# Optimization experiments

Hardware: AMD Instinct MI355X
Metric: run time of the kernel (lower is better)

## Reference

```python
import jax, jax.numpy as jnp
import numpy as np

V, E, H, B, T = 50000, 300, 512, 256, 64
D_OUT = 3
EPS = 1e-5


def setup_inputs() -> dict:
    key = jax.random.key(0)
    ks = jax.random.split(key, 16)
    s = lambda k, shape: (jax.random.normal(k, shape, jnp.float32) * 0.05)
    return {
        "premise": jax.random.randint(ks[0], (T, B), 0, V),
        "hypothesis": jax.random.randint(ks[1], (T, B), 0, V),
        "embed": s(ks[2], (V, E)),
        "W_ih": s(ks[3], (4 * H, E)),
        "W_hh": s(ks[4], (4 * H, H)),
        "b_ih": s(ks[5], (4 * H,)),
        "b_hh": s(ks[6], (4 * H,)),
        "bn0_g": jnp.ones((4 * H,), jnp.float32),
        "bn0_b": jnp.zeros((4 * H,), jnp.float32),
        "W0": s(ks[7], (4 * H, 4 * H)),
        "b0": s(ks[8], (4 * H,)),
        "bn1_g": jnp.ones((4 * H,), jnp.float32),
        "bn1_b": jnp.zeros((4 * H,), jnp.float32),
        "W1": s(ks[9], (4 * H, 4 * H)),
        "b1": s(ks[10], (4 * H,)),
        "bno_g": jnp.ones((4 * H,), jnp.float32),
        "bno_b": jnp.zeros((4 * H,), jnp.float32),
        "Wo": s(ks[11], (D_OUT, 4 * H)),
        "bo": s(ks[12], (D_OUT,)),
    }


def _lstm_final_h(xs, W_ih, W_hh, bias):
    # xs: [T, N, E]; shared-weight LSTMCell scan, returns final hidden [N, H]
    x_proj = jnp.einsum('tne,ge->tng', xs, W_ih) + bias  # hoist input GEMM out of the recurrence
    n = xs.shape[1]
    h0 = jnp.zeros((n, H), xs.dtype)

    def step(carry, xg):
        h, c = carry
        gates = xg + h @ W_hh.T
        i, f, g, o = jnp.split(gates, 4, axis=-1)  # torch LSTMCell gate order
        c = jax.nn.sigmoid(f) * c + jax.nn.sigmoid(i) * jnp.tanh(g)
        h = jax.nn.sigmoid(o) * jnp.tanh(c)
        return (h, c), None

    (h, _), _ = jax.lax.scan(step, (h0, h0), x_proj)
    return h


def _bn(x, g, b):
    # BatchNorm1d in training mode: biased batch stats
    mu = x.mean(0)
    var = x.var(0)
    return (x - mu) * jax.lax.rsqrt(var + EPS) * g + b


def reference(premise, hypothesis, embed, W_ih, W_hh, b_ih, b_hh,
              bn0_g, bn0_b, W0, b0, bn1_g, bn1_b, W1, b1,
              bno_g, bno_b, Wo, bo):
    p = embed[premise]      # [T, B, E]
    hyp = embed[hypothesis]  # [T, B, E]
    combined = jnp.concatenate([p, hyp], axis=1)  # [T, 2B, E]
    bias = b_ih + b_hh
    h_fw = _lstm_final_h(combined, W_ih, W_hh, bias)          # forward direction
    h_bw = _lstm_final_h(combined[::-1], W_ih, W_hh, bias)    # backward direction (shared cell)
    feat = jnp.concatenate([h_fw[:B], h_bw[:B], h_fw[B:], h_bw[B:]], axis=1)  # [B, 4H]
    x = jax.nn.relu(_bn(feat, bn0_g, bn0_b) @ W0.T + b0)
    x = jax.nn.relu(_bn(x, bn1_g, bn1_b) @ W1.T + b1)
    return _bn(x, bno_g, bno_b) @ Wo.T + bo  # [B, d_out]
```

## Files before the change

kernel.cpp:

```cpp
#include <hip/hip_runtime.h>
#include <hip/hip_bf16.h>


typedef __attribute__((ext_vector_type(8))) short bf16x8;
typedef __attribute__((ext_vector_type(4))) float f32x4;
typedef __attribute__((ext_vector_type(2))) unsigned int u32x2;

#define DEVI __device__ __forceinline__

template<int N> struct IC { static constexpr int v = N; };

template<int AUX> DEVI void async16t(const void* g, void* l) {
  __builtin_amdgcn_global_load_lds((const __attribute__((address_space(1))) void*)g,
                                   (__attribute__((address_space(3))) void*)l,
                                   16, 0, AUX);
}
DEVI void async16(const void* g, void* l) { async16t<0>(g, l); }
DEVI u32x2 load8_pin(const void* addr) {
  u32x2 r;
  asm volatile("global_load_dwordx2 %0, %1, off" : "=v"(r) : "v"(addr) : "memory");
  return r;
}
DEVI void storeh_coh(void* a, unsigned int v) {
  asm volatile("global_store_short %0, %1, off sc0 sc1" ::"v"(a), "v"(v) : "memory");
}
template<int N> DEVI void vmwait_barrier() {
  asm volatile("s_waitcnt vmcnt(%0)" ::"i"(N) : "memory");
  __builtin_amdgcn_s_barrier();
  __builtin_amdgcn_sched_barrier(0);
}
DEVI float sigmf_(float x) { return 1.f / (1.f + __expf(-x)); }
DEVI float tanhf_(float x) {
  float a = __expf(-2.f * fabsf(x));
  float t = (1.f - a) / (1.f + a);
  return copysignf(t, x);
}
DEVI __hip_bfloat16 f2b(float x) { return __float2bfloat16(x); }
DEVI float b2f(__hip_bfloat16 x) { return __bfloat162float(x); }

__global__ void cvt_f32_bf16(const float* __restrict__ src,
                             __hip_bfloat16* __restrict__ dst, int n4) {
  int i = blockIdx.x * 256 + threadIdx.x;
  int stride = gridDim.x * 256;
  for (; i < n4; i += stride) {
    float4 v = ((const float4*)src)[i];
    union { __hip_bfloat16 h[4]; uint2 u; } o;
    o.h[0] = f2b(v.x); o.h[1] = f2b(v.y); o.h[2] = f2b(v.z); o.h[3] = f2b(v.w);
    ((uint2*)dst)[i] = o.u;
  }
}

__global__ void pack_wih(const float* __restrict__ W_ih,
                         const float* __restrict__ b_ih,
                         const float* __restrict__ b_hh,
                         __hip_bfloat16* __restrict__ WihP,
                         float* __restrict__ biasL) {
  int tid = blockIdx.x * 256 + threadIdx.x;
  int stride = gridDim.x * 256;
  for (int i = tid; i < 2048 * 320; i += stride) {
    int r = i / 320, c = i - r * 320;
    WihP[i] = (c < 300) ? f2b(W_ih[r * 300 + c]) : f2b(0.f);
  }
  if (tid < 2048) biasL[tid] = b_ih[tid] + b_hh[tid];
}

__global__ void gather_kernel(const int* __restrict__ prem, const int* __restrict__ hyp,
                              const float* __restrict__ embed,
                              __hip_bfloat16* __restrict__ Ain) {
  int row = blockIdx.x * 4 + (threadIdx.x >> 6);
  int lane = threadIdx.x & 63;
  int tt = row >> 9, n = row & 511;
  int tok = (n < 256) ? prem[tt * 256 + n] : hyp[tt * 256 + (n - 256)];
  const float4* e4 = (const float4*)(embed + (size_t)tok * 300);
  uint2* d2 = (uint2*)(Ain + (size_t)row * 320);
  for (int j = lane; j < 75; j += 64) {
    float4 v = e4[j];
    union { __hip_bfloat16 h[4]; uint2 u; } o;
    o.h[0] = f2b(v.x); o.h[1] = f2b(v.y); o.h[2] = f2b(v.z); o.h[3] = f2b(v.w);
    d2[j] = o.u;
  }
  for (int j = 75 + lane; j < 80; j += 64) d2[j] = make_uint2(0u, 0u);
}

template<int BM, int EPI>
__global__ __launch_bounds__(256)
void gemm_pipe(const __hip_bfloat16* __restrict__ A,
               const __hip_bfloat16* __restrict__ Bn,
               const float* __restrict__ bias,
               void* __restrict__ Cout, int K, int ldc) {
  constexpr int BK = 64;
  constexpr int ABYT = BM * BK * 2;
  constexpr int BBYT = 128 * BK * 2;
  constexpr int APW = BM / 32;
  constexpr int IFL = APW + 4;
  constexpr int WM = BM / 2, MT = WM / 16;
  __shared__ alignas(16) char smem[2 * ABYT + 2 * BBYT];

  const int tid = threadIdx.x, lane = tid & 63, wid = tid >> 6;
  const int wrow = wid >> 1, wcol = wid & 1;
  const int m0 = blockIdx.x * BM, n0 = blockIdx.y * 128;
  const int l8 = lane & 7, ld8 = lane >> 3;
  const int swz = (l8 ^ ld8) * 8;

  const __hip_bfloat16* Abase = A + (size_t)m0 * K;
  const __hip_bfloat16* Bbase = Bn + (size_t)n0 * K;

  f32x4 acc[MT][4];
#pragma unroll
  for (int i = 0; i < MT; ++i)
#pragma unroll
    for (int j = 0; j < 4; ++j) acc[i][j] = {0.f, 0.f, 0.f, 0.f};

  auto stage = [&](int buf, int kt) {
    const __hip_bfloat16* as = Abase + kt * BK + swz;
    char* ad = smem + buf * ABYT;
#pragma unroll
    for (int s = 0; s < APW; ++s) {
      int iss = wid * APW + s;
      async16(as + (size_t)(iss * 8 + ld8) * K, ad + iss * 1024);
    }
    const __hip_bfloat16* bs = Bbase + kt * BK + swz;
    char* bd = smem + 2 * ABYT + buf * BBYT;
#pragma unroll
    for (int s = 0; s < 4; ++s) {
      int iss = wid * 4 + s;
      async16(bs + (size_t)(iss * 8 + ld8) * K, bd + iss * 1024);
    }
  };

  const int nk = K / BK;
  stage(0, 0);
  for (int kt = 0; kt < nk; ++kt) {
    if (kt + 1 < nk) {
      stage((kt + 1) & 1, kt + 1);
      vmwait_barrier<IFL>();
    } else {
      vmwait_barrier<0>();
    }
    const __hip_bfloat16* ab = (const __hip_bfloat16*)(smem + (kt & 1) * ABYT);
    const __hip_bfloat16* bb = (const __hip_bfloat16*)(smem + 2 * ABYT + (kt & 1) * BBYT);
#pragma unroll
    for (int kk = 0; kk < BK; kk += 32) {
      bf16x8 af[MT], bf[4];
#pragma unroll
      for (int i = 0; i < MT; ++i) {
        int r = wrow * WM + i * 16 + (lane & 15);
        af[i] = *(const bf16x8*)&ab[r * BK + ((kk + (lane >> 4) * 8) ^ ((r & 7) * 8))];
      }
#pragma unroll
      for (int j = 0; j < 4; ++j) {
        int r = wcol * 64 + j * 16 + (lane & 15);
        bf[j] = *(const bf16x8*)&bb[r * BK + ((kk + (lane >> 4) * 8) ^ ((r & 7) * 8))];
      }
#pragma unroll
      for (int i = 0; i < MT; ++i)
#pragma unroll
        for (int j = 0; j < 4; ++j)
          acc[i][j] = __builtin_amdgcn_mfma_f32_16x16x32_bf16(af[i], bf[j], acc[i][j], 0, 0, 0);
    }
    __builtin_amdgcn_s_barrier();
  }

  if (EPI == 2) {
#pragma unroll
    for (int i = 0; i < MT; ++i)
#pragma unroll
      for (int j = 0; j < 4; ++j) {
        union { __hip_bfloat16 h[4]; uint2 u; } o;
#pragma unroll
        for (int rr = 0; rr < 4; ++rr) o.h[rr] = f2b(acc[i][j][rr]);
        size_t slot = (((size_t)blockIdx.x * 16 + blockIdx.y) * 4 + wid) * 16 + i * 4 + j;
        *(uint2*)((char*)Cout + slot * 512 + lane * 8) = o.u;
      }
    return;
  }

  __syncthreads();
  float* Csm = (float*)smem;
#pragma unroll
  for (int i = 0; i < MT; ++i)
#pragma unroll
    for (int j = 0; j < 4; ++j)
#pragma unroll
      for (int rr = 0; rr < 4; ++rr) {
        int row = wrow * WM + i * 16 + (lane >> 4) * 4 + rr;
        int col = wcol * 64 + j * 16 + (lane & 15);
        Csm[row * 128 + (col ^ ((row & 7) << 2))] = acc[i][j][rr];
      }
  __syncthreads();
#pragma unroll
  for (int it = 0; it < BM / 16; ++it) {
    int idx = it * 256 + tid;
    int row = idx >> 4;
    int cb = (idx & 15) * 8;
    int sw = (row & 7) << 2;
    float4 v0 = *(const float4*)&Csm[row * 128 + (cb ^ sw)];
    float4 v1 = *(const float4*)&Csm[row * 128 + ((cb + 4) ^ sw)];
    float4 b0 = *(const float4*)&bias[n0 + cb];
    float4 b1 = *(const float4*)&bias[n0 + cb + 4];
    v0.x = fmaxf(v0.x + b0.x, 0.f); v0.y = fmaxf(v0.y + b0.y, 0.f);
    v0.z = fmaxf(v0.z + b0.z, 0.f); v0.w = fmaxf(v0.w + b0.w, 0.f);
    v1.x = fmaxf(v1.x + b1.x, 0.f); v1.y = fmaxf(v1.y + b1.y, 0.f);
    v1.z = fmaxf(v1.z + b1.z, 0.f); v1.w = fmaxf(v1.w + b1.w, 0.f);
    size_t base = (size_t)(m0 + row) * ldc + n0 + cb;
    *(float4*)&((float*)Cout)[base] = v0;
    *(float4*)&((float*)Cout)[base + 4] = v1;
  }
}

__global__ __launch_bounds__(256, 2)
void lstm_persist(const __hip_bfloat16* __restrict__ xp,
                  const __hip_bfloat16* __restrict__ Whh,
                  const float* __restrict__ biasL,
                  __hip_bfloat16* __restrict__ hA,
                  __hip_bfloat16* __restrict__ hB,
                  int* __restrict__ ctr) {
  extern __shared__ char smem[];
  const int tid = threadIdx.x, lane = tid & 63, wid = tid >> 6;
  const int bid = blockIdx.x;
  const int grp = (bid & 7) | ((bid >> 8) << 3);
  const int jt2 = (bid >> 3) & 31;
  const int m0 = grp * 64;
  const int l8 = lane & 7, ld8 = lane >> 3;
  const int swz = (l8 ^ ld8) * 8;

  bf16x8 w[16];
  for (int hh = 0; hh < 2; ++hh) {
#pragma unroll
    for (int kt2 = 0; kt2 < 4; ++kt2)
#pragma unroll
      for (int s = 0; s < 2; ++s) {
        int iss = wid * 2 + s;
        int r = iss * 8 + ld8;
        int Wrow = (r >> 4) * 512 + jt2 * 16 + (r & 15);
        async16(Whh + (size_t)Wrow * 512 + (hh * 4 + kt2) * 64 + swz,
                smem + kt2 * 8192 + iss * 1024);
      }
    asm volatile("s_waitcnt vmcnt(0)" ::: "memory");
    __builtin_amdgcn_s_barrier();
    __builtin_amdgcn_sched_barrier(0);
    {
      const __hip_bfloat16* wb = (const __hip_bfloat16*)smem;
      int r = wid * 16 + (lane & 15);
#pragma unroll
      for (int kt2 = 0; kt2 < 4; ++kt2)
#pragma unroll
        for (int kkh = 0; kkh < 2; ++kkh)
          w[(hh * 4 + kt2) * 2 + kkh] =
              *(const bf16x8*)&wb[kt2 * 4096 + r * 64 +
                                  ((kkh * 32 + (lane >> 4) * 8) ^ ((r & 7) * 8))];
    }
    __syncthreads();
  }

  int* flag = (int*)(smem + 49152);
  if (tid == 0) {
    int xcd = (int)(__builtin_amdgcn_s_getreg((31 << 11) | 20) & 15);
    int o1 = atomicOr(&ctr[grp * 64 + 1], 1 << xcd);
    int o2 = atomicOr(&ctr[1025], 1 << xcd);
    asm volatile("" ::"v"(o1), "v"(o2));
    atomicAdd(&ctr[1024], 1);
    while (__hip_atomic_load(&ctr[1024], __ATOMIC_RELAXED, __HIP_MEMORY_SCOPE_AGENT) < 512)
      __builtin_amdgcn_s_sleep(2);
    int gm = __hip_atomic_load(&ctr[grp * 64 + 1], __ATOMIC_RELAXED, __HIP_MEMORY_SCOPE_AGENT);
    int am = __hip_atomic_load(&ctr[1025], __ATOMIC_RELAXED, __HIP_MEMORY_SCOPE_AGENT);
    *flag = (__popc((unsigned)gm) == 1 && __popc((unsigned)am) == 8) ? 1 : 0;
  }
  __syncthreads();
  const bool fastpath = (*flag != 0);
  __syncthreads();

  const int q = lane >> 4, c = lane & 15;
  const int widx = (grp & 1) * 2 + ((jt2 & 7) >> 2);
  const int jx = jt2 & 3;
  const int byb = jt2 >> 3;
  float bias_[4];
#pragma unroll
  for (int g = 0; g < 4; ++g) bias_[g] = biasL[g * 512 + jt2 * 16 + c];

  float c_[4];
#pragma unroll
  for (int e = 0; e < 4; ++e) c_[e] = 0.f;

  auto run = [&](auto FC) {
    constexpr bool FAST = decltype(FC)::v;
    constexpr int AUX = FAST ? 1 : 17;
    for (int t = 0; t < 64; ++t) {
      const __hip_bfloat16* hin = (t & 1) ? hB : hA;
      __hip_bfloat16* hout = (t & 1) ? hA : hB;

      auto issueA = [&](int kt) {
#pragma unroll
        for (int s = 0; s < 2; ++s) {
          int iss = wid * 2 + s;
          async16t<AUX>(hin + (size_t)(m0 + iss * 8 + ld8) * 512 + kt * 64 + swz,
                        smem + (kt & 3) * 8192 + iss * 1024);
        }
      };
      issueA(0); issueA(1); issueA(2);
      __builtin_amdgcn_sched_barrier(0);
      const int xbase = (grp < 8) ? (t * 512 + m0) : ((63 - t) * 512 + (m0 - 512));
      const int bx = xbase >> 7;
      u32x2 xg[4];
#pragma unroll
      for (int g = 0; g < 4; ++g) {
        size_t slot = (((size_t)bx * 16 + g * 4 + byb) * 4 + widx) * 16 + wid * 4 + jx;
        xg[g] = load8_pin((const char*)xp + slot * 512 + lane * 8);
      }
      __builtin_amdgcn_sched_barrier(0);

      f32x4 acc[4];
#pragma unroll
      for (int i = 0; i < 4; ++i) acc[i] = {0.f, 0.f, 0.f, 0.f};

      auto do_kt = [&](auto K) {
        constexpr int KT = decltype(K)::v;
        constexpr int WT[8] = {8, 8, 8, 4, 4, 4, 2, 0};
        vmwait_barrier<WT[KT]>();
        if constexpr (KT < 5) issueA(KT + 3);
        const __hip_bfloat16* ab = (const __hip_bfloat16*)(smem + (KT & 3) * 8192);
#pragma unroll
        for (int kk = 0; kk < 64; kk += 32) {
          bf16x8 af[4];
#pragma unroll
          for (int i = 0; i < 4; ++i) {
            int r = i * 16 + (lane & 15);
            af[i] = *(const bf16x8*)&ab[r * 64 + ((kk + (lane >> 4) * 8) ^ ((r & 7) * 8))];
          }
#pragma unroll
          for (int i = 0; i < 4; ++i)
            acc[i] = __builtin_amdgcn_mfma_f32_16x16x32_bf16(
                af[i], w[KT * 2 + kk / 32], acc[i], 0, 0, 0);
        }
      };
      do_kt(IC<0>{}); do_kt(IC<1>{}); do_kt(IC<2>{}); do_kt(IC<3>{});
      do_kt(IC<4>{}); do_kt(IC<5>{}); do_kt(IC<6>{}); do_kt(IC<7>{});

      float* gsm = (float*)(smem + 32768);
#pragma unroll
      for (int i = 0; i < 4; ++i)
        *(f32x4*)(gsm + (wid * 4 + i) * 256 + lane * 4) = acc[i];
      __syncthreads();
      f32x4 gq[4];
#pragma unroll
      for (int g = 0; g < 4; ++g)
        gq[g] = *(const f32x4*)(gsm + (g * 4 + wid) * 256 + lane * 4);
      asm volatile("s_waitcnt vmcnt(0)" ::: "memory");
      __builtin_amdgcn_sched_barrier(0);

      union { u32x2 v; __hip_bfloat16 h[4]; } X[4];
#pragma unroll
      for (int g = 0; g < 4; ++g) X[g].v = xg[g];
      __hip_bfloat16* hbase = hout + (size_t)(m0 + wid * 16 + q * 4) * 512 + jt2 * 16 + c;
#pragma unroll
      for (int rr = 0; rr < 4; ++rr) {
        float gi = gq[0][rr] + b2f(X[0].h[rr]) + bias_[0];
        float gf = gq[1][rr] + b2f(X[1].h[rr]) + bias_[1];
        float gg = gq[2][rr] + b2f(X[2].h[rr]) + bias_[2];
        float go = gq[3][rr] + b2f(X[3].h[rr]) + bias_[3];
        float cn = sigmf_(gf) * c_[rr] + sigmf_(gi) * tanhf_(gg);
        float hn = sigmf_(go) * tanhf_(cn);
        c_[rr] = cn;
        union { __hip_bfloat16 b; unsigned short u; } hb;
        hb.b = f2b(hn);
        if constexpr (FAST) {
          hbase[rr * 512] = hb.b;
        } else {
          storeh_coh(hbase + rr * 512, (unsigned int)hb.u);
        }
      }
      asm volatile("s_waitcnt vmcnt(0)" ::: "memory");
      __syncthreads();

      if (t < 63) {
        if (tid == 0) {
          const int target = 32 * (t + 1);
          int got = atomicAdd(&ctr[grp * 64], 1) + 1;
          if (got < target) {
            while (__hip_atomic_load(&ctr[grp * 64], __ATOMIC_RELAXED,
                                     __HIP_MEMORY_SCOPE_AGENT) < target)
              __builtin_amdgcn_s_sleep(1);
          }
        }
        __syncthreads();
      }
    }
  };
  if (fastpath) run(IC<1>{});
  else          run(IC<0>{});
}

__global__ void feat_kernel(const __hip_bfloat16* __restrict__ hA, float* __restrict__ feat) {
  int b = blockIdx.x;
  for (int c = threadIdx.x; c < 2048; c += 256) {
    int sec = c >> 9, j = c & 511;
    int row = (sec == 0) ? b : (sec == 1) ? 512 + b : (sec == 2) ? 256 + b : 768 + b;
    feat[b * 2048 + c] = b2f(hA[(size_t)row * 512 + j]);
  }
}

__global__ void bn_stats(const float* __restrict__ x, const float* __restrict__ g,
                         const float* __restrict__ b,
                         float* __restrict__ sc, float* __restrict__ sh) {
  int c = blockIdx.x * 256 + threadIdx.x;
  float s = 0.f, s2 = 0.f;
  for (int r = 0; r < 256; ++r) {
    float v = x[r * 2048 + c];
    s += v;
    s2 += v * v;
  }
  float mu = s * (1.f / 256.f);
  float var = s2 * (1.f / 256.f) - mu * mu;
  float rs = rsqrtf(var + 1e-5f);
  float scale = g[c] * rs;
  sc[c] = scale;
  sh[c] = b[c] - mu * scale;
}

__global__ void bn_apply(const float* __restrict__ x, const float* __restrict__ sc,
                         const float* __restrict__ sh, __hip_bfloat16* __restrict__ xn) {
  int i = blockIdx.x * 256 + threadIdx.x;
  int c = i & 2047;
  xn[i] = f2b(x[i] * sc[c] + sh[c]);
}

__global__ void final_kernel(const float* __restrict__ x2, const float* __restrict__ sc,
                             const float* __restrict__ sh, const float* __restrict__ Wo,
                             const float* __restrict__ bo, float* __restrict__ out) {
  __shared__ float red[3][256];
  int b = blockIdx.x, tid = threadIdx.x;
  float a0 = 0.f, a1 = 0.f, a2 = 0.f;
  for (int c = tid; c < 2048; c += 256) {
    float v = x2[b * 2048 + c] * sc[c] + sh[c];
    a0 += v * Wo[c];
    a1 += v * Wo[2048 + c];
    a2 += v * Wo[4096 + c];
  }
  red[0][tid] = a0; red[1][tid] = a1; red[2][tid] = a2;
  __syncthreads();
  for (int s = 128; s > 0; s >>= 1) {
    if (tid < s) {
      red[0][tid] += red[0][tid + s];
      red[1][tid] += red[1][tid + s];
      red[2][tid] += red[2][tid + s];
    }
    __syncthreads();
  }
  if (tid < 3) out[b * 3 + tid] = red[tid][0] + bo[tid];
}

extern "C" void kernel_launch(void* const* d_in, const int* in_sizes, int n_in,
                              void* d_out, int out_size, void* d_ws, size_t ws_size,
                              hipStream_t stream) {
  (void)in_sizes; (void)n_in; (void)out_size; (void)ws_size;
  const int* prem = (const int*)d_in[0];
  const int* hyp = (const int*)d_in[1];
  const float* embed = (const float*)d_in[2];
  const float* W_ih = (const float*)d_in[3];
  const float* W_hh = (const float*)d_in[4];
  const float* b_ih = (const float*)d_in[5];
  const float* b_hh = (const float*)d_in[6];
  const float* bn0g = (const float*)d_in[7];
  const float* bn0b = (const float*)d_in[8];
  const float* W0 = (const float*)d_in[9];
  const float* b0 = (const float*)d_in[10];
  const float* bn1g = (const float*)d_in[11];
  const float* bn1b = (const float*)d_in[12];
  const float* W1 = (const float*)d_in[13];
  const float* b1 = (const float*)d_in[14];
  const float* bnog = (const float*)d_in[15];
  const float* bnob = (const float*)d_in[16];
  const float* Wo = (const float*)d_in[17];
  const float* bo = (const float*)d_in[18];
  float* out = (float*)d_out;

  char* w = (char*)d_ws;
  size_t off = 0;
  auto alloc = [&](size_t bytes) {
    void* p = w + off;
    off += (bytes + 255) & ~(size_t)255;
    return p;
  };
  __hip_bfloat16* WihP = (__hip_bfloat16*)alloc((size_t)2048 * 320 * 2);
  __hip_bfloat16* Whhb = (__hip_bfloat16*)alloc((size_t)2048 * 512 * 2);
  __hip_bfloat16* W0b = (__hip_bfloat16*)alloc((size_t)2048 * 2048 * 2);
  __hip_bfloat16* W1b = (__hip_bfloat16*)alloc((size_t)2048 * 2048 * 2);
  float* biasL = (float*)alloc(2048 * 4);
  int* ctr = (int*)alloc(2048 * 4);
  __hip_bfloat16* xp = (__hip_bfloat16*)alloc((size_t)32768 * 2048 * 2);
  size_t ain_off = off;
  __hip_bfloat16* Ain = (__hip_bfloat16*)alloc((size_t)32768 * 320 * 2);
  size_t end_off = off;
  off = ain_off;
  __hip_bfloat16* hA = (__hip_bfloat16*)alloc((size_t)1024 * 512 * 2);
  __hip_bfloat16* hB = (__hip_bfloat16*)alloc((size_t)1024 * 512 * 2);
  float* feat = (float*)alloc((size_t)256 * 2048 * 4);
  __hip_bfloat16* xn = (__hip_bfloat16*)alloc((size_t)256 * 2048 * 2);
  float* x1 = (float*)alloc((size_t)256 * 2048 * 4);
  float* x2 = (float*)alloc((size_t)256 * 2048 * 4);
  float* sc0 = (float*)alloc(2048 * 4);
  float* sh0 = (float*)alloc(2048 * 4);
  float* sc1 = (float*)alloc(2048 * 4);
  float* sh1 = (float*)alloc(2048 * 4);
  float* sc2 = (float*)alloc(2048 * 4);
  float* sh2 = (float*)alloc(2048 * 4);
  (void)end_off;

  (void)hipMemsetAsync(ctr, 0, 2048 * 4, stream);
  pack_wih<<<512, 256, 0, stream>>>(W_ih, b_ih, b_hh, WihP, biasL);
  cvt_f32_bf16<<<1024, 256, 0, stream>>>(W_hh, Whhb, 2048 * 512 / 4);
  cvt_f32_bf16<<<2048, 256, 0, stream>>>(W0, W0b, 2048 * 2048 / 4);
  cvt_f32_bf16<<<2048, 256, 0, stream>>>(W1, W1b, 2048 * 2048 / 4);
  gather_kernel<<<8192, 256, 0, stream>>>(prem, hyp, embed, Ain);
  gemm_pipe<128, 2><<<dim3(256, 16), 256, 0, stream>>>(Ain, WihP, biasL, xp, 320, 2048);
  (void)hipMemsetAsync(hA, 0, (size_t)1024 * 512 * 2, stream);
  (void)hipFuncSetAttribute(reinterpret_cast<const void*>(lstm_persist),
                            hipFuncAttributeMaxDynamicSharedMemorySize, 65536);
  lstm_persist<<<512, 256, 49408, stream>>>(xp, Whhb, biasL, hA, hB, ctr);
  feat_kernel<<<256, 256, 0, stream>>>(hA, feat);
  bn_stats<<<8, 256, 0, stream>>>(feat, bn0g, bn0b, sc0, sh0);
  bn_apply<<<2048, 256, 0, stream>>>(feat, sc0, sh0, xn);
  gemm_pipe<64, 1><<<dim3(4, 16), 256, 0, stream>>>(xn, W0b, b0, x1, 2048, 2048);
  bn_stats<<<8, 256, 0, stream>>>(x1, bn1g, bn1b, sc1, sh1);
  bn_apply<<<2048, 256, 0, stream>>>(x1, sc1, sh1, xn);
  gemm_pipe<64, 1><<<dim3(4, 16), 256, 0, stream>>>(xn, W1b, b1, x2, 2048, 2048);
  bn_stats<<<8, 256, 0, stream>>>(x2, bnog, bnob, sc2, sh2);
  final_kernel<<<256, 256, 0, stream>>>(x2, sc2, sh2, Wo, bo, out);
}
```

Before: 471.6 us.

## Interleave forward and backward LSTM chains within each persistent block

Halves the persistent LSTM grid so each block owns the same W_hh tile for both the forward and backward sequence groups. It then software-pipelines the two independent recurrences: while one chain waits on its cross-block step counter, the block prefetches and computes the other chain's step. This hides the barrier and load latency of one recurrence behind the other's work. In exchange it needs more LDS per block, runs at one block per CU, and moves from 512 to 256 blocks, which could cut parallelism if the interleaving does not cover the lost occupancy.

```diff
diff --git a/kernel.cpp b/kernel.cpp
--- a/kernel.cpp
+++ b/kernel.cpp
@@ -208,7 +208,7 @@
   }
 }
 
-__global__ __launch_bounds__(256, 2)
+__global__ __launch_bounds__(256, 1)
 void lstm_persist(const __hip_bfloat16* __restrict__ xp,
                   const __hip_bfloat16* __restrict__ Whh,
                   const float* __restrict__ biasL,
@@ -218,9 +218,8 @@
   extern __shared__ char smem[];
   const int tid = threadIdx.x, lane = tid & 63, wid = tid >> 6;
   const int bid = blockIdx.x;
-  const int grp = (bid & 7) | ((bid >> 8) << 3);
+  const int g = bid & 7;
   const int jt2 = (bid >> 3) & 31;
-  const int m0 = grp * 64;
   const int l8 = lane & 7, ld8 = lane >> 3;
   const int swz = (l8 ^ ld8) * 8;
 
@@ -253,16 +252,16 @@
     __syncthreads();
   }
 
-  int* flag = (int*)(smem + 49152);
+  int* flag = (int*)(smem + 81920);
   if (tid == 0) {
     int xcd = (int)(__builtin_amdgcn_s_getreg((31 << 11) | 20) & 15);
-    int o1 = atomicOr(&ctr[grp * 64 + 1], 1 << xcd);
+    int o1 = atomicOr(&ctr[g * 64 + 1], 1 << xcd);
     int o2 = atomicOr(&ctr[1025], 1 << xcd);
     asm volatile("" ::"v"(o1), "v"(o2));
     atomicAdd(&ctr[1024], 1);
-    while (__hip_atomic_load(&ctr[1024], __ATOMIC_RELAXED, __HIP_MEMORY_SCOPE_AGENT) < 512)
+    while (__hip_atomic_load(&ctr[1024], __ATOMIC_RELAXED, __HIP_MEMORY_SCOPE_AGENT) < 256)
       __builtin_amdgcn_s_sleep(2);
-    int gm = __hip_atomic_load(&ctr[grp * 64 + 1], __ATOMIC_RELAXED, __HIP_MEMORY_SCOPE_AGENT);
+    int gm = __hip_atomic_load(&ctr[g * 64 + 1], __ATOMIC_RELAXED, __HIP_MEMORY_SCOPE_AGENT);
     int am = __hip_atomic_load(&ctr[1025], __ATOMIC_RELAXED, __HIP_MEMORY_SCOPE_AGENT);
     *flag = (__popc((unsigned)gm) == 1 && __popc((unsigned)am) == 8) ? 1 : 0;
   }
@@ -271,54 +270,85 @@
   __syncthreads();
 
   const int q = lane >> 4, c = lane & 15;
-  const int widx = (grp & 1) * 2 + ((jt2 & 7) >> 2);
+  const int widx = (g & 1) * 2 + ((jt2 & 7) >> 2);
   const int jx = jt2 & 3;
   const int byb = jt2 >> 3;
   float bias_[4];
 #pragma unroll
-  for (int g = 0; g < 4; ++g) bias_[g] = biasL[g * 512 + jt2 * 16 + c];
-
-  float c_[4];
-#pragma unroll
-  for (int e = 0; e < 4; ++e) c_[e] = 0.f;
+  for (int gg = 0; gg < 4; ++gg) bias_[gg] = biasL[gg * 512 + jt2 * 16 + c];
+
+  float c0_[4], c1_[4];
+#pragma unroll
+  for (int e = 0; e < 4; ++e) { c0_[e] = 0.f; c1_[e] = 0.f; }
+  u32x2 xg0_[4], xg1_[4];
 
   auto run = [&](auto FC) {
     constexpr bool FAST = decltype(FC)::v;
     constexpr int AUX = FAST ? 1 : 17;
-    for (int t = 0; t < 64; ++t) {
+
+    auto WOP = [&](int grpIdx, int t) {
+      if (tid == 0) {
+        const int target = 32 * (t + 1);
+        if (__hip_atomic_load(&ctr[grpIdx * 64], __ATOMIC_RELAXED,
+                              __HIP_MEMORY_SCOPE_AGENT) < target) {
+          while (__hip_atomic_load(&ctr[grpIdx * 64], __ATOMIC_RELAXED,
+                                   __HIP_MEMORY_SCOPE_AGENT) < target)
+            __builtin_amdgcn_s_sleep(1);
+        }
+      }
+      __syncthreads();
+    };
+
+    auto IOP = [&](auto CC, int t) {
+      constexpr int ch = decltype(CC)::v;
+      const int mm0 = ch ? (512 + g * 64) : (g * 64);
+      const __hip_bfloat16* hin = (t & 1) ? hB : hA;
+      char* abase = smem + ch * 32768;
+#pragma unroll
+      for (int kt = 0; kt < 3; ++kt)
+#pragma unroll
+        for (int s = 0; s < 2; ++s) {
+          int iss = wid * 2 + s;
+          async16t<AUX>(hin + (size_t)(mm0 + iss * 8 + ld8) * 512 + kt * 64 + swz,
+                        abase + kt * 8192 + iss * 1024);
+        }
+      __builtin_amdgcn_sched_barrier(0);
+      const int xbase = ch ? ((63 - t) * 512 + g * 64) : (t * 512 + g * 64);
+      const int bx = xbase >> 7;
+      u32x2(&xg)[4] = ch ? xg1_ : xg0_;
+#pragma unroll
+      for (int gg = 0; gg < 4; ++gg) {
+        size_t slot = (((size_t)bx * 16 + gg * 4 + byb) * 4 + widx) * 16 + wid * 4 + jx;
+        xg[gg] = load8_pin((const char*)xp + slot * 512 + lane * 8);
+      }
+      __builtin_amdgcn_sched_barrier(0);
+    };
+
+    auto CBODY = [&](auto CC, int t) {
+      constexpr int ch = decltype(CC)::v;
+      const int mm0 = ch ? (512 + g * 64) : (g * 64);
+      const int grpIdx = ch ? (8 + g) : g;
       const __hip_bfloat16* hin = (t & 1) ? hB : hA;
       __hip_bfloat16* hout = (t & 1) ? hA : hB;
-
+      char* abase = smem + ch * 32768;
       auto issueA = [&](int kt) {
 #pragma unroll
         for (int s = 0; s < 2; ++s) {
           int iss = wid * 2 + s;
-          async16t<AUX>(hin + (size_t)(m0 + iss * 8 + ld8) * 512 + kt * 64 + swz,
-                        smem + (kt & 3) * 8192 + iss * 1024);
+          async16t<AUX>(hin + (size_t)(mm0 + iss * 8 + ld8) * 512 + kt * 64 + swz,
+                        abase + (kt & 3) * 8192 + iss * 1024);
         }
       };
-      issueA(0); issueA(1); issueA(2);
-      __builtin_amdgcn_sched_barrier(0);
-      const int xbase = (grp < 8) ? (t * 512 + m0) : ((63 - t) * 512 + (m0 - 512));
-      const int bx = xbase >> 7;
-      u32x2 xg[4];
-#pragma unroll
-      for (int g = 0; g < 4; ++g) {
-        size_t slot = (((size_t)bx * 16 + g * 4 + byb) * 4 + widx) * 16 + wid * 4 + jx;
-        xg[g] = load8_pin((const char*)xp + slot * 512 + lane * 8);
-      }
-      __builtin_amdgcn_sched_barrier(0);
-
       f32x4 acc[4];
 #pragma unroll
       for (int i = 0; i < 4; ++i) acc[i] = {0.f, 0.f, 0.f, 0.f};
 
       auto do_kt = [&](auto K) {
         constexpr int KT = decltype(K)::v;
-        constexpr int WT[8] = {8, 8, 8, 4, 4, 4, 2, 0};
+        constexpr int WT[8] = {18, 18, 18, 4, 4, 4, 2, 0};
         vmwait_barrier<WT[KT]>();
         if constexpr (KT < 5) issueA(KT + 3);
-        const __hip_bfloat16* ab = (const __hip_bfloat16*)(smem + (KT & 3) * 8192);
+        const __hip_bfloat16* ab = (const __hip_bfloat16*)(abase + (KT & 3) * 8192);
 #pragma unroll
         for (int kk = 0; kk < 64; kk += 32) {
           bf16x8 af[4];
@@ -336,31 +366,31 @@
       do_kt(IC<0>{}); do_kt(IC<1>{}); do_kt(IC<2>{}); do_kt(IC<3>{});
       do_kt(IC<4>{}); do_kt(IC<5>{}); do_kt(IC<6>{}); do_kt(IC<7>{});
 
-      float* gsm = (float*)(smem + 32768);
+      float* gsm = (float*)(smem + 65536);
 #pragma unroll
       for (int i = 0; i < 4; ++i)
         *(f32x4*)(gsm + (wid * 4 + i) * 256 + lane * 4) = acc[i];
       __syncthreads();
       f32x4 gq[4];
 #pragma unroll
-      for (int g = 0; g < 4; ++g)
-        gq[g] = *(const f32x4*)(gsm + (g * 4 + wid) * 256 + lane * 4);
-      asm volatile("s_waitcnt vmcnt(0)" ::: "memory");
-      __builtin_amdgcn_sched_barrier(0);
-
+      for (int gg = 0; gg < 4; ++gg)
+        gq[gg] = *(const f32x4*)(gsm + (gg * 4 + wid) * 256 + lane * 4);
+
+      u32x2(&xg)[4] = ch ? xg1_ : xg0_;
+      float(&cs)[4] = ch ? c1_ : c0_;
       union { u32x2 v; __hip_bfloat16 h[4]; } X[4];
 #pragma unroll
-      for (int g = 0; g < 4; ++g) X[g].v = xg[g];
-      __hip_bfloat16* hbase = hout + (size_t)(m0 + wid * 16 + q * 4) * 512 + jt2 * 16 + c;
+      for (int gg = 0; gg < 4; ++gg) X[gg].v = xg[gg];
+      __hip_bfloat16* hbase = hout + (size_t)(mm0 + wid * 16 + q * 4) * 512 + jt2 * 16 + c;
 #pragma unroll
       for (int rr = 0; rr < 4; ++rr) {
         float gi = gq[0][rr] + b2f(X[0].h[rr]) + bias_[0];
         float gf = gq[1][rr] + b2f(X[1].h[rr]) + bias_[1];
-        float gg = gq[2][rr] + b2f(X[2].h[rr]) + bias_[2];
+        float gg2 = gq[2][rr] + b2f(X[2].h[rr]) + bias_[2];
         float go = gq[3][rr] + b2f(X[3].h[rr]) + bias_[3];
-        float cn = sigmf_(gf) * c_[rr] + sigmf_(gi) * tanhf_(gg);
+        float cn = sigmf_(gf) * cs[rr] + sigmf_(gi) * tanhf_(gg2);
         float hn = sigmf_(go) * tanhf_(cn);
-        c_[rr] = cn;
+        cs[rr] = cn;
         union { __hip_bfloat16 b; unsigned short u; } hb;
         hb.b = f2b(hn);
         if constexpr (FAST) {
@@ -371,20 +401,22 @@
       }
       asm volatile("s_waitcnt vmcnt(0)" ::: "memory");
       __syncthreads();
-
-      if (t < 63) {
-        if (tid == 0) {
-          const int target = 32 * (t + 1);
-          int got = atomicAdd(&ctr[grp * 64], 1) + 1;
-          if (got < target) {
-            while (__hip_atomic_load(&ctr[grp * 64], __ATOMIC_RELAXED,
-                                     __HIP_MEMORY_SCOPE_AGENT) < target)
-              __builtin_amdgcn_s_sleep(1);
-          }
-        }
-        __syncthreads();
-      }
-    }
+      if (tid == 0) atomicAdd(&ctr[grpIdx * 64], 1);
+    };
+
+    IOP(IC<0>{}, 0);
+    IOP(IC<1>{}, 0);
+    CBODY(IC<0>{}, 0);
+    for (int t = 1; t < 64; ++t) {
+      WOP(g, t - 1);
+      IOP(IC<0>{}, t);
+      CBODY(IC<1>{}, t - 1);
+      WOP(8 + g, t - 1);
+      IOP(IC<1>{}, t);
+      CBODY(IC<0>{}, t);
+    }
+    WOP(8 + g, 62);
+    CBODY(IC<1>{}, 63);
   };
   if (fastpath) run(IC<1>{});
   else          run(IC<0>{});
@@ -515,8 +547,8 @@
   gemm_pipe<128, 2><<<dim3(256, 16), 256, 0, stream>>>(Ain, WihP, biasL, xp, 320, 2048);
   (void)hipMemsetAsync(hA, 0, (size_t)1024 * 512 * 2, stream);
   (void)hipFuncSetAttribute(reinterpret_cast<const void*>(lstm_persist),
-                            hipFuncAttributeMaxDynamicSharedMemorySize, 65536);
-  lstm_persist<<<512, 256, 49408, stream>>>(xp, Whhb, biasL, hA, hB, ctr);
+                            hipFuncAttributeMaxDynamicSharedMemorySize, 98304);
+  lstm_persist<<<256, 256, 82176, stream>>>(xp, Whhb, biasL, hA, hB, ctr);
   feat_kernel<<<256, 256, 0, stream>>>(hA, feat);
   bn_stats<<<8, 256, 0, stream>>>(feat, bn0g, bn0b, sc0, sh0);
   bn_apply<<<2048, 256, 0, stream>>>(feat, sc0, sh0, xn);
```

Result: slower. 588.7 us (+24.8%).

## Fuse input projection into persistent LSTM recurrence and use per-block step flags

Applied to the files above, without the earlier changes.

Removes the separate x@W_ih GEMM and its large bf16 xp buffer. The persistent LSTM kernel now keeps W_ih slices resident in registers alongside W_hh and streams the gathered embeddings each step, so every step runs 13 K-tiles instead of 8. The group barrier changes from a shared atomic counter to per-block step flags polled by one wavefront. This saves roughly 128MB of xp write and read traffic, but adds MFMA work and register pressure inside the latency-bound serial recurrence.

```diff
diff --git a/kernel.cpp b/kernel.cpp
--- a/kernel.cpp
+++ b/kernel.cpp
@@ -4,7 +4,6 @@
 
 typedef __attribute__((ext_vector_type(8))) short bf16x8;
 typedef __attribute__((ext_vector_type(4))) float f32x4;
-typedef __attribute__((ext_vector_type(2))) unsigned int u32x2;
 
 #define DEVI __device__ __forceinline__
 
@@ -16,11 +15,6 @@
                                    16, 0, AUX);
 }
 DEVI void async16(const void* g, void* l) { async16t<0>(g, l); }
-DEVI u32x2 load8_pin(const void* addr) {
-  u32x2 r;
-  asm volatile("global_load_dwordx2 %0, %1, off" : "=v"(r) : "v"(addr) : "memory");
-  return r;
-}
 DEVI void storeh_coh(void* a, unsigned int v) {
   asm volatile("global_store_short %0, %1, off sc0 sc1" ::"v"(a), "v"(v) : "memory");
 }
@@ -82,12 +76,12 @@
   for (int j = 75 + lane; j < 80; j += 64) d2[j] = make_uint2(0u, 0u);
 }
 
-template<int BM, int EPI>
+template<int BM>
 __global__ __launch_bounds__(256)
-void gemm_pipe(const __hip_bfloat16* __restrict__ A,
+void gemm_relu(const __hip_bfloat16* __restrict__ A,
                const __hip_bfloat16* __restrict__ Bn,
                const float* __restrict__ bias,
-               void* __restrict__ Cout, int K, int ldc) {
+               float* __restrict__ Cout, int K, int ldc) {
   constexpr int BK = 64;
   constexpr int ABYT = BM * BK * 2;
   constexpr int BBYT = 128 * BK * 2;
@@ -159,20 +153,6 @@
           acc[i][j] = __builtin_amdgcn_mfma_f32_16x16x32_bf16(af[i], bf[j], acc[i][j], 0, 0, 0);
     }
     __builtin_amdgcn_s_barrier();
-  }
-
-  if (EPI == 2) {
-#pragma unroll
-    for (int i = 0; i < MT; ++i)
-#pragma unroll
-      for (int j = 0; j < 4; ++j) {
-        union { __hip_bfloat16 h[4]; uint2 u; } o;
-#pragma unroll
-        for (int rr = 0; rr < 4; ++rr) o.h[rr] = f2b(acc[i][j][rr]);
-        size_t slot = (((size_t)blockIdx.x * 16 + blockIdx.y) * 4 + wid) * 16 + i * 4 + j;
-        *(uint2*)((char*)Cout + slot * 512 + lane * 8) = o.u;
-      }
-    return;
   }
 
   __syncthreads();
@@ -203,14 +183,15 @@
     v1.x = fmaxf(v1.x + b1.x, 0.f); v1.y = fmaxf(v1.y + b1.y, 0.f);
     v1.z = fmaxf(v1.z + b1.z, 0.f); v1.w = fmaxf(v1.w + b1.w, 0.f);
     size_t base = (size_t)(m0 + row) * ldc + n0 + cb;
-    *(float4*)&((float*)Cout)[base] = v0;
-    *(float4*)&((float*)Cout)[base + 4] = v1;
+    *(float4*)&Cout[base] = v0;
+    *(float4*)&Cout[base + 4] = v1;
   }
 }
 
 __global__ __launch_bounds__(256, 2)
-void lstm_persist(const __hip_bfloat16* __restrict__ xp,
+void lstm_persist(const __hip_bfloat16* __restrict__ Ain,
                   const __hip_bfloat16* __restrict__ Whh,
+                  const __hip_bfloat16* __restrict__ Wih,
                   const float* __restrict__ biasL,
                   __hip_bfloat16* __restrict__ hA,
                   __hip_bfloat16* __restrict__ hB,
@@ -224,18 +205,26 @@
   const int l8 = lane & 7, ld8 = lane >> 3;
   const int swz = (l8 ^ ld8) * 8;
 
-  bf16x8 w[16];
-  for (int hh = 0; hh < 2; ++hh) {
-#pragma unroll
-    for (int kt2 = 0; kt2 < 4; ++kt2)
+  bf16x8 w_[26];
+#pragma unroll
+  for (int rnd = 0; rnd < 4; ++rnd) {
+    const int nc = (rnd == 3) ? 1 : 4;
+#pragma unroll
+    for (int ci = 0; ci < 4; ++ci) {
+      if (ci >= nc) continue;
+      int kt = rnd * 4 + ci;
+      const __hip_bfloat16* src = (kt < 8) ? Whh : Wih;
+      const int stride = (kt < 8) ? 512 : 320;
+      const int coloff = (kt < 8) ? kt * 64 : (kt - 8) * 64;
 #pragma unroll
       for (int s = 0; s < 2; ++s) {
         int iss = wid * 2 + s;
         int r = iss * 8 + ld8;
         int Wrow = (r >> 4) * 512 + jt2 * 16 + (r & 15);
-        async16(Whh + (size_t)Wrow * 512 + (hh * 4 + kt2) * 64 + swz,
-                smem + kt2 * 8192 + iss * 1024);
-      }
+        async16(src + (size_t)Wrow * stride + coloff + swz,
+                smem + ci * 8192 + iss * 1024);
+      }
+    }
     asm volatile("s_waitcnt vmcnt(0)" ::: "memory");
     __builtin_amdgcn_s_barrier();
     __builtin_amdgcn_sched_barrier(0);
@@ -243,12 +232,15 @@
       const __hip_bfloat16* wb = (const __hip_bfloat16*)smem;
       int r = wid * 16 + (lane & 15);
 #pragma unroll
-      for (int kt2 = 0; kt2 < 4; ++kt2)
+      for (int ci = 0; ci < 4; ++ci) {
+        if (ci >= nc) continue;
+        int kt = rnd * 4 + ci;
 #pragma unroll
         for (int kkh = 0; kkh < 2; ++kkh)
-          w[(hh * 4 + kt2) * 2 + kkh] =
-              *(const bf16x8*)&wb[kt2 * 4096 + r * 64 +
+          w_[kt * 2 + kkh] =
+              *(const bf16x8*)&wb[ci * 4096 + r * 64 +
                                   ((kkh * 32 + (lane >> 4) * 8) ^ ((r & 7) * 8))];
+      }
     }
     __syncthreads();
   }
@@ -256,14 +248,14 @@
   int* flag = (int*)(smem + 49152);
   if (tid == 0) {
     int xcd = (int)(__builtin_amdgcn_s_getreg((31 << 11) | 20) & 15);
-    int o1 = atomicOr(&ctr[grp * 64 + 1], 1 << xcd);
-    int o2 = atomicOr(&ctr[1025], 1 << xcd);
+    int o1 = atomicOr(&ctr[512 + grp], 1 << xcd);
+    int o2 = atomicOr(&ctr[545], 1 << xcd);
     asm volatile("" ::"v"(o1), "v"(o2));
-    atomicAdd(&ctr[1024], 1);
-    while (__hip_atomic_load(&ctr[1024], __ATOMIC_RELAXED, __HIP_MEMORY_SCOPE_AGENT) < 512)
+    atomicAdd(&ctr[544], 1);
+    while (__hip_atomic_load(&ctr[544], __ATOMIC_RELAXED, __HIP_MEMORY_SCOPE_AGENT) < 512)
       __builtin_amdgcn_s_sleep(2);
-    int gm = __hip_atomic_load(&ctr[grp * 64 + 1], __ATOMIC_RELAXED, __HIP_MEMORY_SCOPE_AGENT);
-    int am = __hip_atomic_load(&ctr[1025], __ATOMIC_RELAXED, __HIP_MEMORY_SCOPE_AGENT);
+    int gm = __hip_atomic_load(&ctr[512 + grp], __ATOMIC_RELAXED, __HIP_MEMORY_SCOPE_AGENT);
+    int am = __hip_atomic_load(&ctr[545], __ATOMIC_RELAXED, __HIP_MEMORY_SCOPE_AGENT);
     *flag = (__popc((unsigned)gm) == 1 && __popc((unsigned)am) == 8) ? 1 : 0;
   }
   __syncthreads();
@@ -271,12 +263,9 @@
   __syncthreads();
 
   const int q = lane >> 4, c = lane & 15;
-  const int widx = (grp & 1) * 2 + ((jt2 & 7) >> 2);
-  const int jx = jt2 & 3;
-  const int byb = jt2 >> 3;
   float bias_[4];
 #pragma unroll
-  for (int g = 0; g < 4; ++g) bias_[g] = biasL[g * 512 + jt2 * 16 + c];
+  for (int gg = 0; gg < 4; ++gg) bias_[gg] = biasL[gg * 512 + jt2 * 16 + c];
 
   float c_[4];
 #pragma unroll
@@ -288,26 +277,23 @@
     for (int t = 0; t < 64; ++t) {
       const __hip_bfloat16* hin = (t & 1) ? hB : hA;
       __hip_bfloat16* hout = (t & 1) ? hA : hB;
+      const int xrow = (grp < 8) ? (t * 512 + m0) : ((63 - t) * 512 + (m0 - 512));
 
       auto issueA = [&](int kt) {
 #pragma unroll
         for (int s = 0; s < 2; ++s) {
           int iss = wid * 2 + s;
-          async16t<AUX>(hin + (size_t)(m0 + iss * 8 + ld8) * 512 + kt * 64 + swz,
-                        smem + (kt & 3) * 8192 + iss * 1024);
+          if (kt < 8) {
+            async16t<AUX>(hin + (size_t)(m0 + iss * 8 + ld8) * 512 + kt * 64 + swz,
+                          smem + (kt & 3) * 8192 + iss * 1024);
+          } else {
+            async16(Ain + (size_t)(xrow + iss * 8 + ld8) * 320 + (kt - 8) * 64 + swz,
+                    smem + (kt & 3) * 8192 + iss * 1024);
+          }
         }
       };
       issueA(0); issueA(1); issueA(2);
       __builtin_amdgcn_sched_barrier(0);
-      const int xbase = (grp < 8) ? (t * 512 + m0) : ((63 - t) * 512 + (m0 - 512));
-      const int bx = xbase >> 7;
-      u32x2 xg[4];
-#pragma unroll
-      for (int g = 0; g < 4; ++g) {
-        size_t slot = (((size_t)bx * 16 + g * 4 + byb) * 4 + widx) * 16 + wid * 4 + jx;
-        xg[g] = load8_pin((const char*)xp + slot * 512 + lane * 8);
-      }
-      __builtin_amdgcn_sched_barrier(0);
 
       f32x4 acc[4];
 #pragma unroll
@@ -315,9 +301,9 @@
 
       auto do_kt = [&](auto K) {
         constexpr int KT = decltype(K)::v;
-        constexpr int WT[8] = {8, 8, 8, 4, 4, 4, 2, 0};
+        constexpr int WT[13] = {4, 4, 4, 4, 4, 4, 4, 4, 4, 4, 4, 2, 0};
         vmwait_barrier<WT[KT]>();
-        if constexpr (KT < 5) issueA(KT + 3);
+        if constexpr (KT < 10) issueA(KT + 3);
         const __hip_bfloat16* ab = (const __hip_bfloat16*)(smem + (KT & 3) * 8192);
 #pragma unroll
         for (int kk = 0; kk < 64; kk += 32) {
@@ -330,11 +316,13 @@
 #pragma unroll
           for (int i = 0; i < 4; ++i)
             acc[i] = __builtin_amdgcn_mfma_f32_16x16x32_bf16(
-                af[i], w[KT * 2 + kk / 32], acc[i], 0, 0, 0);
+                af[i], w_[KT * 2 + kk / 32], acc[i], 0, 0, 0);
         }
       };
       do_kt(IC<0>{}); do_kt(IC<1>{}); do_kt(IC<2>{}); do_kt(IC<3>{});
       do_kt(IC<4>{}); do_kt(IC<5>{}); do_kt(IC<6>{}); do_kt(IC<7>{});
+      do_kt(IC<8>{}); do_kt(IC<9>{}); do_kt(IC<10>{}); do_kt(IC<11>{});
+      do_kt(IC<12>{});
 
       float* gsm = (float*)(smem + 32768);
 #pragma unroll
@@ -343,22 +331,17 @@
       __syncthreads();
       f32x4 gq[4];
 #pragma unroll
-      for (int g = 0; g < 4; ++g)
-        gq[g] = *(const f32x4*)(gsm + (g * 4 + wid) * 256 + lane * 4);
-      asm volatile("s_waitcnt vmcnt(0)" ::: "memory");
-      __builtin_amdgcn_sched_barrier(0);
-
-      union { u32x2 v; __hip_bfloat16 h[4]; } X[4];
-#pragma unroll
-      for (int g = 0; g < 4; ++g) X[g].v = xg[g];
+      for (int gg = 0; gg < 4; ++gg)
+        gq[gg] = *(const f32x4*)(gsm + (gg * 4 + wid) * 256 + lane * 4);
+
       __hip_bfloat16* hbase = hout + (size_t)(m0 + wid * 16 + q * 4) * 512 + jt2 * 16 + c;
 #pragma unroll
       for (int rr = 0; rr < 4; ++rr) {
-        float gi = gq[0][rr] + b2f(X[0].h[rr]) + bias_[0];
-        float gf = gq[1][rr] + b2f(X[1].h[rr]) + bias_[1];
-        float gg = gq[2][rr] + b2f(X[2].h[rr]) + bias_[2];
-        float go = gq[3][rr] + b2f(X[3].h[rr]) + bias_[3];
-        float cn = sigmf_(gf) * c_[rr] + sigmf_(gi) * tanhf_(gg);
+        float gi = gq[0][rr] + bias_[0];
+        float gf = gq[1][rr] + bias_[1];
+        float gg2 = gq[2][rr] + bias_[2];
+        float go = gq[3][rr] + bias_[3];
+        float cn = sigmf_(gf) * c_[rr] + sigmf_(gi) * tanhf_(gg2);
         float hn = sigmf_(go) * tanhf_(cn);
         c_[rr] = cn;
         union { __hip_bfloat16 b; unsigned short u; } hb;
@@ -373,14 +356,20 @@
       __syncthreads();
 
       if (t < 63) {
-        if (tid == 0) {
-          const int target = 32 * (t + 1);
-          int got = atomicAdd(&ctr[grp * 64], 1) + 1;
-          if (got < target) {
-            while (__hip_atomic_load(&ctr[grp * 64], __ATOMIC_RELAXED,
-                                     __HIP_MEMORY_SCOPE_AGENT) < target)
-              __builtin_amdgcn_s_sleep(1);
-          }
+        if (wid == 0) {
+          const int target = t + 1;
+          if (tid == 0)
+            __hip_atomic_store(&ctr[grp * 32 + jt2], target, __ATOMIC_RELAXED,
+                               __HIP_MEMORY_SCOPE_AGENT);
+          bool ok;
+          do {
+            int v = (lane < 32)
+                        ? __hip_atomic_load(&ctr[grp * 32 + lane], __ATOMIC_RELAXED,
+                                            __HIP_MEMORY_SCOPE_AGENT)
+                        : target;
+            ok = __all(v >= target);
+            if (!ok) __builtin_amdgcn_s_sleep(1);
+          } while (!ok);
         }
         __syncthreads();
       }
@@ -486,12 +475,8 @@
   __hip_bfloat16* W0b = (__hip_bfloat16*)alloc((size_t)2048 * 2048 * 2);
   __hip_bfloat16* W1b = (__hip_bfloat16*)alloc((size_t)2048 * 2048 * 2);
   float* biasL = (float*)alloc(2048 * 4);
-  int* ctr = (int*)alloc(2048 * 4);
-  __hip_bfloat16* xp = (__hip_bfloat16*)alloc((size_t)32768 * 2048 * 2);
-  size_t ain_off = off;
+  int* ctr = (int*)alloc(1024 * 4);
   __hip_bfloat16* Ain = (__hip_bfloat16*)alloc((size_t)32768 * 320 * 2);
-  size_t end_off = off;
-  off = ain_off;
   __hip_bfloat16* hA = (__hip_bfloat16*)alloc((size_t)1024 * 512 * 2);
   __hip_bfloat16* hB = (__hip_bfloat16*)alloc((size_t)1024 * 512 * 2);
   float* feat = (float*)alloc((size_t)256 * 2048 * 4);
@@ -504,26 +489,24 @@
   float* sh1 = (float*)alloc(2048 * 4);
   float* sc2 = (float*)alloc(2048 * 4);
   float* sh2 = (float*)alloc(2048 * 4);
-  (void)end_off;
-
-  (void)hipMemsetAsync(ctr, 0, 2048 * 4, stream);
+
+  (void)hipMemsetAsync(ctr, 0, 1024 * 4, stream);
+  (void)hipMemsetAsync(hA, 0, (size_t)1024 * 512 * 2, stream);
   pack_wih<<<512, 256, 0, stream>>>(W_ih, b_ih, b_hh, WihP, biasL);
   cvt_f32_bf16<<<1024, 256, 0, stream>>>(W_hh, Whhb, 2048 * 512 / 4);
+  gather_kernel<<<8192, 256, 0, stream>>>(prem, hyp, embed, Ain);
+  (void)hipFuncSetAttribute(reinterpret_cast<const void*>(lstm_persist),
+                            hipFuncAttributeMaxDynamicSharedMemorySize, 65536);
+  lstm_persist<<<512, 256, 49408, stream>>>(Ain, Whhb, WihP, biasL, hA, hB, ctr);
   cvt_f32_bf16<<<2048, 256, 0, stream>>>(W0, W0b, 2048 * 2048 / 4);
   cvt_f32_bf16<<<2048, 256, 0, stream>>>(W1, W1b, 2048 * 2048 / 4);
-  gather_kernel<<<8192, 256, 0, stream>>>(prem, hyp, embed, Ain);
-  gemm_pipe<128, 2><<<dim3(256, 16), 256, 0, stream>>>(Ain, WihP, biasL, xp, 320, 2048);
-  (void)hipMemsetAsync(hA, 0, (size_t)1024 * 512 * 2, stream);
-  (void)hipFuncSetAttribute(reinterpret_cast<const void*>(lstm_persist),
-                            hipFuncAttributeMaxDynamicSharedMemorySize, 65536);
-  lstm_persist<<<512, 256, 49408, stream>>>(xp, Whhb, biasL, hA, hB, ctr);
   feat_kernel<<<256, 256, 0, stream>>>(hA, feat);
   bn_stats<<<8, 256, 0, stream>>>(feat, bn0g, bn0b, sc0, sh0);
   bn_apply<<<2048, 256, 0, stream>>>(feat, sc0, sh0, xn);
-  gemm_pipe<64, 1><<<dim3(4, 16), 256, 0, stream>>>(xn, W0b, b0, x1, 2048, 2048);
+  gemm_relu<64><<<dim3(4, 16), 256, 0, stream>>>(xn, W0b, b0, x1, 2048, 2048);
   bn_stats<<<8, 256, 0, stream>>>(x1, bn1g, bn1b, sc1, sh1);
   bn_apply<<<2048, 256, 0, stream>>>(x1, sc1, sh1, xn);
-  gemm_pipe<64, 1><<<dim3(4, 16), 256, 0, stream>>>(xn, W1b, b1, x2, 2048, 2048);
+  gemm_relu<64><<<dim3(4, 16), 256, 0, stream>>>(xn, W1b, b1, x2, 2048, 2048);
   bn_stats<<<8, 256, 0, stream>>>(x2, bnog, bnob, sc2, sh2);
   final_kernel<<<256, 256, 0, stream>>>(x2, sc2, sh2, Wo, bo, out);
 }
```

New measurement: 512.6 us. 8.7% more time.
